# Kernel tuning notes

Measured on AMD Instinct MI355X. Metric: run time of the kernel, lower is better.

Reference implementation:

```python
import jax, jax.numpy as jnp
import numpy as np
from jax import lax

D_MODEL = 1024
N_HEADS = 8
D_HEAD = 64
D_INNER = N_HEADS * D_HEAD  # 512
B, T = 4, 4096
LN_EPS = 1e-5
NORM_EPS = 1e-12  # F.normalize default eps


def setup_inputs() -> dict:
    key = jax.random.key(0)
    ks = jax.random.split(key, 6)
    s_proj = (2.0 / (D_MODEL + D_INNER)) ** 0.5  # xavier_uniform-ish std
    x = jax.random.normal(ks[0], (B, T, D_MODEL), jnp.float32)
    Wq = jax.random.normal(ks[1], (D_MODEL, D_INNER), jnp.float32) * s_proj
    Wk = jax.random.normal(ks[2], (D_MODEL, D_INNER), jnp.float32) * s_proj
    Wv = jax.random.normal(ks[3], (D_MODEL, D_INNER), jnp.float32) * s_proj
    Wa = jax.random.normal(ks[4], (D_MODEL, D_INNER), jnp.float32) * s_proj
    ba = jnp.full((D_INNER,), 3.0, jnp.float32)  # nn.init.constant_(W_alpha.bias, 3.0)
    Wo = jax.random.normal(ks[5], (D_INNER, D_MODEL), jnp.float32) * s_proj
    gamma = jnp.ones((D_MODEL,), jnp.float32)
    beta = jnp.zeros((D_MODEL,), jnp.float32)
    return {"x": x, "Wq": Wq, "Wk": Wk, "Wv": Wv, "Wa": Wa, "ba": ba,
            "Wo": Wo, "gamma": gamma, "beta": beta}


def reference(x, Wq, Wk, Wv, Wa, ba, Wo, gamma, beta):
    Bx, Tx, _ = x.shape
    residual = x
    # LayerNorm
    mu = jnp.mean(x, axis=-1, keepdims=True)
    var = jnp.var(x, axis=-1, keepdims=True)
    xn = (x - mu) / jnp.sqrt(var + LN_EPS) * gamma + beta
    # Projections -> (B, T, H, d) -> time-major (T, B, H, d) for scan
    def heads(y):
        return jnp.moveaxis(y.reshape(Bx, Tx, N_HEADS, D_HEAD), 1, 0)
    q = heads(xn @ Wq)
    k = heads(xn @ Wk)
    v = heads(xn @ Wv)
    alpha = jax.nn.sigmoid(heads(xn @ Wa + ba))
    # F.normalize(k, dim=-1)
    knorm = jnp.linalg.norm(k, axis=-1, keepdims=True)
    k = k / jnp.maximum(knorm, NORM_EPS)

    # Recurrence: S_t = diag(a_t) S_{t-1} + k_t v_t^T ; o_t = S_t^T q_t
    def step(S, inp):
        q_t, k_t, v_t, a_t = inp  # each (B, H, d)
        S = a_t[..., None] * S + k_t[..., None] * v_t[..., None, :]  # (B,H,dk,dv)
        o_t = jnp.einsum('bhji,bhj->bhi', S, q_t)
        return S, o_t

    S0 = jnp.zeros((Bx, N_HEADS, D_HEAD, D_HEAD), x.dtype)
    _, outs = lax.scan(step, S0, (q, k, v, alpha))  # outs: (T, B, H, d)
    out = jnp.moveaxis(outs, 0, 1).reshape(Bx, Tx, D_INNER) @ Wo
    return out + residual
```

## Files before the change

kernel.cpp:

```cpp
#include <hip/hip_runtime.h>
#include <stdint.h>

#define NTOK   16384
#define DM     1024
#define DI     512
#define NH     8
#define DH     64
#define CHUNK  64
#define NCH    64
#define NBHC   2048

using short8 = __attribute__((ext_vector_type(8))) short;
using f32x4  = __attribute__((ext_vector_type(4))) float;

__device__ __forceinline__ unsigned short f2bf(float f) {
  union { float f; unsigned int u; } x; x.f = f;
  unsigned int u = x.u;
  return (unsigned short)((u + 0x7fffu + ((u >> 16) & 1u)) >> 16);
}
__device__ __forceinline__ float bf2f(unsigned short h) {
  union { unsigned int u; float f; } x; x.u = ((unsigned int)h) << 16; return x.f;
}

typedef const __attribute__((address_space(1))) void* gp1_t;
typedef __attribute__((address_space(3))) void* lp3_t;
__device__ __forceinline__ void gload_lds16(const void* g, void* l) {
  __builtin_amdgcn_global_load_lds((gp1_t)g, (lp3_t)l, 16, 0, 0);
}

__global__ __launch_bounds__(256) void init_kernel(const float* __restrict__ x,
                                                   const float* __restrict__ gamma,
                                                   const float* __restrict__ beta,
                                                   const float* __restrict__ Wq,
                                                   const float* __restrict__ Wk,
                                                   const float* __restrict__ Wv,
                                                   const float* __restrict__ Wa,
                                                   const float* __restrict__ Wo,
                                                   unsigned short* __restrict__ xn,
                                                   unsigned short* __restrict__ Wt,
                                                   unsigned short* __restrict__ Wot) {
  const int blk = blockIdx.x, tid = threadIdx.x;
  __shared__ float tile[32][33];
  __shared__ float rs_[4], rss_[4];
  if (blk < NTOK) {
    const int row = blk;
    float4 v = ((const float4*)(x + (long)row * DM))[tid];
    float s  = v.x + v.y + v.z + v.w;
    float ss = v.x * v.x + v.y * v.y + v.z * v.z + v.w * v.w;
    #pragma unroll
    for (int off = 32; off > 0; off >>= 1) { s += __shfl_down(s, off); ss += __shfl_down(ss, off); }
    int wave = tid >> 6, lane = tid & 63;
    if (lane == 0) { rs_[wave] = s; rss_[wave] = ss; }
    __syncthreads();
    s  = rs_[0] + rs_[1] + rs_[2] + rs_[3];
    ss = rss_[0] + rss_[1] + rss_[2] + rss_[3];
    float mu   = s * (1.f / DM);
    float var  = ss * (1.f / DM) - mu * mu;
    float rstd = rsqrtf(var + 1e-5f);
    int idx = tid * 4;
    float xv[4] = {v.x, v.y, v.z, v.w};
    unsigned short o[4];
    #pragma unroll
    for (int j = 0; j < 4; ++j) o[j] = f2bf((xv[j] - mu) * rstd * gamma[idx + j] + beta[idx + j]);
    uint2 pk; pk.x = (unsigned)o[0] | ((unsigned)o[1] << 16); pk.y = (unsigned)o[2] | ((unsigned)o[3] << 16);
    *(uint2*)(xn + (long)row * DM + idx) = pk;
  } else if (blk < NTOK + 2048) {
    const int id = blk - NTOK;
    const int z = id >> 9, r9 = id & 511;
    const float* in = (z == 0) ? Wq : (z == 1) ? Wk : (z == 2) ? Wv : Wa;
    unsigned short* o = Wt + (size_t)z * 512 * 1024;
    int bx = (r9 & 15) * 32, by = (r9 >> 4) * 32;
    int tx = tid & 31, ty = tid >> 5;
    #pragma unroll
    for (int r = ty; r < 32; r += 8) tile[r][tx] = in[(long)(by + r) * 512 + bx + tx];
    __syncthreads();
    #pragma unroll
    for (int r = ty; r < 32; r += 8) o[(long)(bx + r) * 1024 + by + tx] = f2bf(tile[tx][r]);
  } else {
    const int id = blk - NTOK - 2048;
    int bx = (id & 31) * 32, by = (id >> 5) * 32;
    int tx = tid & 31, ty = tid >> 5;
    #pragma unroll
    for (int r = ty; r < 32; r += 8) tile[r][tx] = Wo[(long)(by + r) * 1024 + bx + tx];
    __syncthreads();
    #pragma unroll
    for (int r = ty; r < 32; r += 8) Wot[(long)(bx + r) * 512 + by + tx] = f2bf(tile[tx][r]);
  }
}

#define EPS 136
template <int MODE>
__global__ __launch_bounds__(512) void gemm_bt(const unsigned short* __restrict__ A,
                                               const unsigned short* __restrict__ Bt,
                                               unsigned short* __restrict__ Cb,
                                               float* __restrict__ Cf,
                                               const float* __restrict__ resid,
                                               int M, int N, int K) {
  __shared__ __align__(16) unsigned short smem[128 * EPS];
  unsigned short* As = smem;
  unsigned short* Bs = smem + 8192;
  const int tid = threadIdx.x;
  const int wave = tid >> 6, lane = tid & 63;
  const int quad = lane >> 4, l16 = lane & 15;

  const int Nt = gridDim.y;
  int id = blockIdx.x + blockIdx.y * gridDim.x;
  int group = id / (4 * Nt);
  int rem = id - group * (4 * Nt);
  const int m0 = (group * 4 + (rem & 3)) * 256;
  const int n0 = (rem >> 2) * 128;
  const int wm = (wave & 3) * 64, wn = (wave >> 2) * 64;

  const int r4 = tid >> 2, p4 = (tid & 3) * 8;
  const unsigned short* Ag0 = A + (long)(m0 + r4) * K + p4;
  const unsigned short* Ag1 = A + (long)(m0 + 128 + r4) * K + p4;
  const unsigned short* Bg0 = Bt + (long)(n0 + r4) * K + p4;

  f32x4 acc[4][4];
  #pragma unroll
  for (int i = 0; i < 4; ++i)
    #pragma unroll
    for (int j = 0; j < 4; ++j) acc[i][j] = (f32x4){0.f, 0.f, 0.f, 0.f};

  for (int k0 = 0; k0 < K; k0 += 32) {
    __syncthreads();
    gload_lds16(Ag0 + k0, &As[tid * 8]);
    gload_lds16(Ag1 + k0, &As[(tid + 512) * 8]);
    gload_lds16(Bg0 + k0, &Bs[tid * 8]);
    __syncthreads();
    short8 a[4], b[4];
    #pragma unroll
    for (int mt = 0; mt < 4; ++mt) a[mt] = *(const short8*)&As[(wm + mt * 16 + l16) * 32 + quad * 8];
    #pragma unroll
    for (int nt = 0; nt < 4; ++nt) b[nt] = *(const short8*)&Bs[(wn + nt * 16 + l16) * 32 + quad * 8];
    #pragma unroll
    for (int mt = 0; mt < 4; ++mt)
      #pragma unroll
      for (int nt = 0; nt < 4; ++nt)
        acc[mt][nt] = __builtin_amdgcn_mfma_f32_16x16x32_bf16(a[mt], b[nt], acc[mt][nt], 0, 0, 0);
  }
  unsigned short* epi = smem;
  const int mypass = (wave & 3) >> 1;
  const int rloc = ((wave & 1) * 64);
  #pragma unroll
  for (int h = 0; h < 2; ++h) {
    __syncthreads();
    if (mypass == h) {
      #pragma unroll
      for (int mt = 0; mt < 4; ++mt)
        #pragma unroll
        for (int nt = 0; nt < 4; ++nt)
          #pragma unroll
          for (int r = 0; r < 4; ++r)
            epi[(rloc + mt * 16 + quad * 4 + r) * EPS + wn + nt * 16 + l16] = f2bf(acc[mt][nt][r]);
    }
    __syncthreads();
    if (MODE == 0) {
      #pragma unroll
      for (int i = tid; i < 2048; i += 512) {
        int row = i >> 4, cc = (i & 15) * 8;
        uint4 v = *(const uint4*)&epi[row * EPS + cc];
        *(uint4*)&Cb[(long)(m0 + h * 128 + row) * N + n0 + cc] = v;
      }
    } else {
      #pragma unroll
      for (int i = tid; i < 4096; i += 512) {
        int row = i >> 5, cc = (i & 31) * 4;
        long g = (long)(m0 + h * 128 + row) * N + n0 + cc;
        float4 rv = *(const float4*)&resid[g];
        uint2 pv = *(const uint2*)&epi[row * EPS + cc];
        float4 ov;
        ov.x = bf2f((unsigned short)(pv.x & 0xffffu)) + rv.x;
        ov.y = bf2f((unsigned short)(pv.x >> 16))     + rv.y;
        ov.z = bf2f((unsigned short)(pv.y & 0xffffu)) + rv.z;
        ov.w = bf2f((unsigned short)(pv.y >> 16))     + rv.w;
        *(float4*)&Cf[g] = ov;
      }
    }
  }
}

#define TS 72
__global__ __launch_bounds__(256) void prep_intra_kernel(const unsigned short* __restrict__ Cb,
                                                         const float* __restrict__ ba,
                                                         unsigned short* __restrict__ qt,
                                                         float* __restrict__ Dvec,
                                                         unsigned short* __restrict__ Ointra,
                                                         unsigned short* __restrict__ Tt) {
  const int bhc = blockIdx.x;
  const int c = bhc & 63, bh = bhc >> 6;
  const int h = bh & 7, b = bh >> 3;
  const int tid = threadIdx.x;
  __shared__ __align__(16) unsigned short Qb[4096], Kb[4096], Vb[4096], lamB[4096];
  __shared__ __align__(16) unsigned short Vt[64 * TS], Kt[64 * TS];
  __shared__ float rnF[64], lendF[64];
  const long rowbase = ((long)(b * 4096 + c * 64)) * 2048;
  const int hoff = h * 64;

  if (tid < 64) rnF[tid] = 0.f;
  __syncthreads();

  #pragma unroll
  for (int chunk = 0; chunk < 2; ++chunk) {
    int u = chunk * 256 + tid;
    int t = u >> 3, p = u & 7;
    long g = rowbase + (long)t * 2048 + hoff + p * 8;
    uint4 q4 = *(const uint4*)(Cb + g);
    uint4 k4 = *(const uint4*)(Cb + g + 512);
    uint4 v4 = *(const uint4*)(Cb + g + 1024);
    uint4 a4 = *(const uint4*)(Cb + g + 1536);
    *(uint4*)&Qb[u * 8] = q4;
    *(uint4*)&Kb[u * 8] = k4;
    *(uint4*)&Vb[u * 8] = v4;
    const unsigned short* as_ = (const unsigned short*)&a4;
    unsigned short al[8];
    #pragma unroll
    for (int j = 0; j < 8; ++j) {
      float z = bf2f(as_[j]) + ba[hoff + p * 8 + j];
      al[j] = f2bf(1.f / (1.f + __expf(-z)));
    }
    uint4 pa;
    pa.x = (unsigned)al[0] | ((unsigned)al[1] << 16); pa.y = (unsigned)al[2] | ((unsigned)al[3] << 16);
    pa.z = (unsigned)al[4] | ((unsigned)al[5] << 16); pa.w = (unsigned)al[6] | ((unsigned)al[7] << 16);
    *(uint4*)&lamB[u * 8] = pa;
    const unsigned short* ks = (const unsigned short*)&k4;
    float ssq = 0.f;
    #pragma unroll
    for (int j = 0; j < 8; ++j) { float kv = bf2f(ks[j]); ssq += kv * kv; }
    atomicAdd(&rnF[t], ssq);
  }
  __syncthreads();

  if (tid < 64) {
    int d = tid; float cum = 1.f;
    #pragma unroll
    for (int t = 0; t < 64; ++t) {
      cum *= bf2f(lamB[t * 64 + d]);
      lamB[t * 64 + d] = f2bf(cum);
    }
    Dvec[(long)bhc * 64 + d] = cum;
    lendF[d] = cum;
  } else if (tid < 128) {
    int t = tid - 64;
    rnF[t] = 1.f / fmaxf(sqrtf(rnF[t]), 1e-12f);
  }
  __syncthreads();

  #pragma unroll
  for (int j = 0; j < 16; ++j) {
    int e = j * 256 + tid;
    int t = e >> 6;
    float lam = bf2f(lamB[e]);
    float kn = bf2f(Kb[e]) * rnF[t];
    Qb[e] = f2bf(bf2f(Qb[e]) * lam);
    Kb[e] = f2bf(kn / lam);
  }
  __syncthreads();

  {
    const long obase = (long)bhc * 4096;
    uint4* gq = (uint4*)(qt + obase);
    const uint4* lq = (const uint4*)Qb;
    gq[tid] = lq[tid]; gq[tid + 256] = lq[tid + 256];
  }

  const long base = (long)bhc * 4096;
  const int wave = tid >> 6, lane = tid & 63, quad = lane >> 4, l16 = lane & 15;
  const int mrow = wave * 16 + l16;
  unsigned short* Ps = lamB;

  union { short8 v; short s[8]; } aI;
  aI.v = (short8){0,0,0,0,0,0,0,0};
  {
    int target = ((wave & 1) * 16 + l16) - quad * 8;
    if (target >= 0 && target < 8) aI.s[target] = (short)0x3F80;
  }
  const int bsel = (wave >> 1) * 32;

  {
    short8 a0 = *(const short8*)&Qb[mrow * 64 + quad * 8];
    short8 a1 = *(const short8*)&Qb[mrow * 64 + 32 + quad * 8];
    #pragma unroll
    for (int nt = 0; nt < 4; ++nt) {
      short8 b0 = *(const short8*)&Kb[(nt * 16 + l16) * 64 + quad * 8];
      short8 b1 = *(const short8*)&Kb[(nt * 16 + l16) * 64 + 32 + quad * 8];
      f32x4 acc = (f32x4){0.f, 0.f, 0.f, 0.f};
      acc = __builtin_amdgcn_mfma_f32_16x16x32_bf16(a0, b0, acc, 0, 0, 0);
      acc = __builtin_amdgcn_mfma_f32_16x16x32_bf16(a1, b1, acc, 0, 0, 0);
      #pragma unroll
      for (int r = 0; r < 4; ++r) {
        int t = wave * 16 + quad * 4 + r, u = nt * 16 + l16;
        Ps[t * 64 + u] = (u <= t) ? f2bf(acc[r]) : (unsigned short)0;
      }
    }
  }
  #pragma unroll
  for (int nt = 0; nt < 4; ++nt) {
    short8 bv = *(const short8*)&Vb[(nt * 16 + l16) * 64 + bsel + quad * 8];
    short8 bk = *(const short8*)&Kb[(nt * 16 + l16) * 64 + bsel + quad * 8];
    f32x4 av = (f32x4){0.f, 0.f, 0.f, 0.f};
    f32x4 ak = (f32x4){0.f, 0.f, 0.f, 0.f};
    av = __builtin_amdgcn_mfma_f32_16x16x32_bf16(aI.v, bv, av, 0, 0, 0);
    ak = __builtin_amdgcn_mfma_f32_16x16x32_bf16(aI.v, bk, ak, 0, 0, 0);
    #pragma unroll
    for (int r = 0; r < 4; ++r) {
      int i = wave * 16 + quad * 4 + r, t = nt * 16 + l16;
      Vt[i * TS + t] = f2bf(av[r]);
      Kt[i * TS + t] = f2bf(ak[r]);
    }
  }
  __syncthreads();

  {
    short8 a0 = *(const short8*)&Ps[mrow * 64 + quad * 8];
    short8 a1 = *(const short8*)&Ps[mrow * 64 + 32 + quad * 8];
    #pragma unroll
    for (int nt = 0; nt < 4; ++nt) {
      short8 b0 = *(const short8*)&Vt[(nt * 16 + l16) * TS + quad * 8];
      short8 b1 = *(const short8*)&Vt[(nt * 16 + l16) * TS + 32 + quad * 8];
      f32x4 acc = (f32x4){0.f, 0.f, 0.f, 0.f};
      acc = __builtin_amdgcn_mfma_f32_16x16x32_bf16(a0, b0, acc, 0, 0, 0);
      acc = __builtin_amdgcn_mfma_f32_16x16x32_bf16(a1, b1, acc, 0, 0, 0);
      #pragma unroll
      for (int r = 0; r < 4; ++r) {
        int t = wave * 16 + quad * 4 + r, i = nt * 16 + l16;
        Ointra[base + t * 64 + i] = f2bf(acc[r]);
      }
    }
  }
  {
    short8 a0 = *(const short8*)&Vt[mrow * TS + quad * 8];
    short8 a1 = *(const short8*)&Vt[mrow * TS + 32 + quad * 8];
    #pragma unroll
    for (int nt = 0; nt < 4; ++nt) {
      short8 b0 = *(const short8*)&Kt[(nt * 16 + l16) * TS + quad * 8];
      short8 b1 = *(const short8*)&Kt[(nt * 16 + l16) * TS + 32 + quad * 8];
      f32x4 acc = (f32x4){0.f, 0.f, 0.f, 0.f};
      acc = __builtin_amdgcn_mfma_f32_16x16x32_bf16(a0, b0, acc, 0, 0, 0);
      acc = __builtin_amdgcn_mfma_f32_16x16x32_bf16(a1, b1, acc, 0, 0, 0);
      float le = lendF[nt * 16 + l16];
      #pragma unroll
      for (int r = 0; r < 4; ++r) {
        int i = wave * 16 + quad * 4 + r, j = nt * 16 + l16;
        Tt[base + i * 64 + j] = f2bf(acc[r] * le);
      }
    }
  }
}

__global__ __launch_bounds__(256) void scan_kernel(const unsigned short* __restrict__ Tt,
                                                   const float* __restrict__ Dvec,
                                                   unsigned short* __restrict__ Sst) {
  const int bh = blockIdx.x;
  const int e = blockIdx.y * 256 + threadIdx.x;
  const int j = e & 63;
  float S = 0.f;
  for (int c = 0; c < 64; ++c) {
    const long idx = ((long)(bh * 64 + c)) * 4096 + e;
    const float dj = Dvec[((long)(bh * 64 + c)) * 64 + j];
    Sst[idx] = f2bf(S);
    S = dj * S + bf2f(Tt[idx]);
  }
}

__global__ __launch_bounds__(256) void combine_kernel(const unsigned short* __restrict__ qt,
                                                      const unsigned short* __restrict__ Sst,
                                                      const unsigned short* __restrict__ Ointra,
                                                      unsigned short* __restrict__ O) {
  const int bhc = blockIdx.x;
  const int c = bhc & 63, bh = bhc >> 6;
  const int h = bh & 7, b = bh >> 3;
  const long base = (long)bhc * 4096;
  __shared__ __align__(16) unsigned short Qs[4096], Sb[4096];
  const int tid = threadIdx.x;
  {
    const uint4* gq = (const uint4*)(qt + base);  uint4* lq = (uint4*)Qs;
    const uint4* gs = (const uint4*)(Sst + base); uint4* ls = (uint4*)Sb;
    lq[tid] = gq[tid]; lq[tid + 256] = gq[tid + 256];
    ls[tid] = gs[tid]; ls[tid + 256] = gs[tid + 256];
  }
  __syncthreads();
  const int wave = tid >> 6, lane = tid & 63, quad = lane >> 4, l16 = lane & 15;
  const int mrow = wave * 16 + l16;
  short8 a0 = *(const short8*)&Qs[mrow * 64 + quad * 8];
  short8 a1 = *(const short8*)&Qs[mrow * 64 + 32 + quad * 8];
  #pragma unroll
  for (int nt = 0; nt < 4; ++nt) {
    f32x4 acc;
    #pragma unroll
    for (int r = 0; r < 4; ++r) {
      int t = wave * 16 + quad * 4 + r, i = nt * 16 + l16;
      acc[r] = bf2f(Ointra[base + t * 64 + i]);
    }
    short8 b0 = *(const short8*)&Sb[(nt * 16 + l16) * 64 + quad * 8];
    short8 b1 = *(const short8*)&Sb[(nt * 16 + l16) * 64 + 32 + quad * 8];
    acc = __builtin_amdgcn_mfma_f32_16x16x32_bf16(a0, b0, acc, 0, 0, 0);
    acc = __builtin_amdgcn_mfma_f32_16x16x32_bf16(a1, b1, acc, 0, 0, 0);
    #pragma unroll
    for (int r = 0; r < 4; ++r) {
      int t = wave * 16 + quad * 4 + r, i = nt * 16 + l16;
      O[((long)(b * 4096 + c * 64 + t)) * 512 + h * 64 + i] = f2bf(acc[r]);
    }
  }
}

extern "C" void kernel_launch(void* const* d_in, const int* in_sizes, int n_in,
                              void* d_out, int out_size, void* d_ws, size_t ws_size,
                              hipStream_t stream) {
  const float* x     = (const float*)d_in[0];
  const float* Wq    = (const float*)d_in[1];
  const float* Wk    = (const float*)d_in[2];
  const float* Wv    = (const float*)d_in[3];
  const float* Wa    = (const float*)d_in[4];
  const float* ba    = (const float*)d_in[5];
  const float* Wo    = (const float*)d_in[6];
  const float* gamma = (const float*)d_in[7];
  const float* beta  = (const float*)d_in[8];
  float* out = (float*)d_out;

  char* ws = (char*)d_ws;
  const size_t KB = 1024;
  unsigned short* Wt     = (unsigned short*)(ws + 0 * KB);
  unsigned short* Wot    = (unsigned short*)(ws + 4096 * KB);
  float*          Dvec   = (float*)         (ws + 5120 * KB);
  unsigned short* qt     = (unsigned short*)(ws + 5632 * KB);
  unsigned short* Ttb    = (unsigned short*)(ws + 22016 * KB);
  unsigned short* Sst    = (unsigned short*)(ws + 38400 * KB);
  unsigned short* xn     = (unsigned short*)(ws + 54784 * KB);
  unsigned short* Ointra = (unsigned short*)(ws + 54784 * KB);
  unsigned short* Ob     = (unsigned short*)(ws + 71168 * KB);
  unsigned short* Cb     = (unsigned short*)(ws + 87552 * KB);

  init_kernel<<<NTOK + 2048 + 512, 256, 0, stream>>>(x, gamma, beta, Wq, Wk, Wv, Wa, Wo, xn, Wt, Wot);
  gemm_bt<0><<<dim3(NTOK / 256, 2048 / 128), 512, 0, stream>>>(xn, Wt, Cb, nullptr, nullptr, NTOK, 2048, 1024);
  prep_intra_kernel<<<NBHC, 256, 0, stream>>>(Cb, ba, qt, Dvec, Ointra, Ttb);
  scan_kernel<<<dim3(32, 16), 256, 0, stream>>>(Ttb, Dvec, Sst);
  combine_kernel<<<NBHC, 256, 0, stream>>>(qt, Sst, Ointra, Ob);
  gemm_bt<1><<<dim3(NTOK / 256, 1024 / 128), 512, 0, stream>>>(Ob, Wot, nullptr, out, x, NTOK, 1024, 512);
}
```

Baseline: 308.4 us.

## Replace GEMM with 256x256 double-buffered swizzled-LDS pipelined MFMA kernel

```diff
diff --git a/kernel.cpp b/kernel.cpp
--- a/kernel.cpp
+++ b/kernel.cpp
@@ -88,87 +88,175 @@
   }
 }
 
-#define EPS 136
+#define EPSW 264
 template <int MODE>
-__global__ __launch_bounds__(512) void gemm_bt(const unsigned short* __restrict__ A,
-                                               const unsigned short* __restrict__ Bt,
-                                               unsigned short* __restrict__ Cb,
-                                               float* __restrict__ Cf,
-                                               const float* __restrict__ resid,
-                                               int M, int N, int K) {
-  __shared__ __align__(16) unsigned short smem[128 * EPS];
-  unsigned short* As = smem;
-  unsigned short* Bs = smem + 8192;
+__global__ __launch_bounds__(512, 2) void gemm8(const unsigned short* __restrict__ A,
+                                                const unsigned short* __restrict__ Bt,
+                                                unsigned short* __restrict__ Cb,
+                                                float* __restrict__ Cf,
+                                                const float* __restrict__ resid,
+                                                int M, int N, int K) {
+  __shared__ __align__(16) unsigned short sm[65536];
   const int tid = threadIdx.x;
   const int wave = tid >> 6, lane = tid & 63;
   const int quad = lane >> 4, l16 = lane & 15;
-
-  const int Nt = gridDim.y;
-  int id = blockIdx.x + blockIdx.y * gridDim.x;
-  int group = id / (4 * Nt);
-  int rem = id - group * (4 * Nt);
-  const int m0 = (group * 4 + (rem & 3)) * 256;
-  const int n0 = (rem >> 2) * 128;
-  const int wm = (wave & 3) * 64, wn = (wave >> 2) * 64;
-
-  const int r4 = tid >> 2, p4 = (tid & 3) * 8;
-  const unsigned short* Ag0 = A + (long)(m0 + r4) * K + p4;
-  const unsigned short* Ag1 = A + (long)(m0 + 128 + r4) * K + p4;
-  const unsigned short* Bg0 = Bt + (long)(n0 + r4) * K + p4;
-
-  f32x4 acc[4][4];
-  #pragma unroll
-  for (int i = 0; i < 4; ++i)
+  const int wm = wave >> 2, wn = wave & 3;
+
+  const int nwg = gridDim.x;
+  const int cpx = nwg >> 3;
+  const int bid = blockIdx.x;
+  const int swz = (bid & 7) * cpx + (bid >> 3);
+  const int m0 = (swz & 63) * 256;
+  const int n0 = (swz >> 6) * 256;
+
+  const int rloc = tid >> 3;
+  const int cbu = ((((tid & 7) << 4) ^ ((rloc & 7) << 4)) >> 1);
+  const unsigned short* ap = A + (long)(m0 + rloc) * K + cbu;
+  const unsigned short* bp = Bt + (long)(n0 + rloc) * K + cbu;
+  const int dst = tid * 8;
+
+  const int colu0 = (((quad << 4) ^ ((l16 & 7) << 4)) >> 1);
+  const int colu1 = colu0 ^ 32;
+  const int aoff = (wm * 128 + l16) * 64;
+  const int boff = 16384 + (wn * 64 + l16) * 64;
+
+  f32x4 acc[8][4];
+  #pragma unroll
+  for (int i = 0; i < 8; ++i)
     #pragma unroll
     for (int j = 0; j < 4; ++j) acc[i][j] = (f32x4){0.f, 0.f, 0.f, 0.f};
 
-  for (int k0 = 0; k0 < K; k0 += 32) {
-    __syncthreads();
-    gload_lds16(Ag0 + k0, &As[tid * 8]);
-    gload_lds16(Ag1 + k0, &As[(tid + 512) * 8]);
-    gload_lds16(Bg0 + k0, &Bs[tid * 8]);
-    __syncthreads();
-    short8 a[4], b[4];
-    #pragma unroll
-    for (int mt = 0; mt < 4; ++mt) a[mt] = *(const short8*)&As[(wm + mt * 16 + l16) * 32 + quad * 8];
-    #pragma unroll
-    for (int nt = 0; nt < 4; ++nt) b[nt] = *(const short8*)&Bs[(wn + nt * 16 + l16) * 32 + quad * 8];
+  const int NT = K >> 6;
+
+  #pragma unroll
+  for (int u = 0; u < 4; ++u) {
+    gload_lds16(ap + (long)u * 64 * K, &sm[u * 4096 + dst]);
+    gload_lds16(bp + (long)u * 64 * K, &sm[16384 + u * 4096 + dst]);
+  }
+  asm volatile("s_waitcnt vmcnt(0)" ::: "memory");
+  __builtin_amdgcn_s_barrier();
+  __builtin_amdgcn_sched_barrier(0);
+
+  short8 aR[4][2];
+  short8 bR[2][2][2];
+
+  for (int t = 0; t < NT; ++t) {
+    const unsigned short* sc = sm + (t & 1) * 32768;
+    unsigned short* sn = sm + ((t + 1) & 1) * 32768;
+    const unsigned short* apn = ap + (long)(t + 1) * 64;
+    const unsigned short* bpn = bp + (long)(t + 1) * 64;
+    const bool more = (t + 1 < NT);
+
+    #pragma unroll
+    for (int mt = 0; mt < 4; ++mt) {
+      aR[mt][0] = *(const short8*)&sc[aoff + mt * 1024 + colu0];
+      aR[mt][1] = *(const short8*)&sc[aoff + mt * 1024 + colu1];
+    }
+    #pragma unroll
+    for (int nt = 0; nt < 2; ++nt) {
+      bR[0][nt][0] = *(const short8*)&sc[boff + nt * 1024 + colu0];
+      bR[0][nt][1] = *(const short8*)&sc[boff + nt * 1024 + colu1];
+    }
+    if (more) {
+      gload_lds16(apn,                  &sn[dst]);
+      gload_lds16(apn + (long) 64 * K,  &sn[4096 + dst]);
+      gload_lds16(apn + (long)128 * K,  &sn[8192 + dst]);
+      gload_lds16(apn + (long)192 * K,  &sn[12288 + dst]);
+    }
+    __builtin_amdgcn_s_barrier();
+    __builtin_amdgcn_s_setprio(1);
     #pragma unroll
     for (int mt = 0; mt < 4; ++mt)
       #pragma unroll
-      for (int nt = 0; nt < 4; ++nt)
-        acc[mt][nt] = __builtin_amdgcn_mfma_f32_16x16x32_bf16(a[mt], b[nt], acc[mt][nt], 0, 0, 0);
-  }
-  unsigned short* epi = smem;
-  const int mypass = (wave & 3) >> 1;
-  const int rloc = ((wave & 1) * 64);
+      for (int nt = 0; nt < 2; ++nt) {
+        acc[mt][nt] = __builtin_amdgcn_mfma_f32_16x16x32_bf16(aR[mt][0], bR[0][nt][0], acc[mt][nt], 0, 0, 0);
+        acc[mt][nt] = __builtin_amdgcn_mfma_f32_16x16x32_bf16(aR[mt][1], bR[0][nt][1], acc[mt][nt], 0, 0, 0);
+      }
+    __builtin_amdgcn_s_setprio(0);
+    __builtin_amdgcn_s_barrier();
+
+    #pragma unroll
+    for (int nt = 0; nt < 2; ++nt) {
+      bR[1][nt][0] = *(const short8*)&sc[boff + (nt + 2) * 1024 + colu0];
+      bR[1][nt][1] = *(const short8*)&sc[boff + (nt + 2) * 1024 + colu1];
+    }
+    if (more) {
+      gload_lds16(bpn,                  &sn[16384 + dst]);
+      gload_lds16(bpn + (long) 64 * K,  &sn[16384 + 4096 + dst]);
+      gload_lds16(bpn + (long)128 * K,  &sn[16384 + 8192 + dst]);
+      gload_lds16(bpn + (long)192 * K,  &sn[16384 + 12288 + dst]);
+    }
+    __builtin_amdgcn_s_barrier();
+    __builtin_amdgcn_s_setprio(1);
+    #pragma unroll
+    for (int mt = 0; mt < 4; ++mt)
+      #pragma unroll
+      for (int nt = 0; nt < 2; ++nt) {
+        acc[mt][nt + 2] = __builtin_amdgcn_mfma_f32_16x16x32_bf16(aR[mt][0], bR[1][nt][0], acc[mt][nt + 2], 0, 0, 0);
+        acc[mt][nt + 2] = __builtin_amdgcn_mfma_f32_16x16x32_bf16(aR[mt][1], bR[1][nt][1], acc[mt][nt + 2], 0, 0, 0);
+      }
+    __builtin_amdgcn_s_setprio(0);
+    __builtin_amdgcn_s_barrier();
+
+    #pragma unroll
+    for (int mt = 0; mt < 4; ++mt) {
+      aR[mt][0] = *(const short8*)&sc[aoff + 4096 + mt * 1024 + colu0];
+      aR[mt][1] = *(const short8*)&sc[aoff + 4096 + mt * 1024 + colu1];
+    }
+    __builtin_amdgcn_s_barrier();
+    __builtin_amdgcn_s_setprio(1);
+    #pragma unroll
+    for (int mt = 0; mt < 4; ++mt)
+      #pragma unroll
+      for (int nt = 0; nt < 2; ++nt) {
+        acc[4 + mt][nt + 2] = __builtin_amdgcn_mfma_f32_16x16x32_bf16(aR[mt][0], bR[1][nt][0], acc[4 + mt][nt + 2], 0, 0, 0);
+        acc[4 + mt][nt + 2] = __builtin_amdgcn_mfma_f32_16x16x32_bf16(aR[mt][1], bR[1][nt][1], acc[4 + mt][nt + 2], 0, 0, 0);
+      }
+    __builtin_amdgcn_s_setprio(0);
+    __builtin_amdgcn_s_barrier();
+
+    __builtin_amdgcn_s_barrier();
+    __builtin_amdgcn_s_setprio(1);
+    #pragma unroll
+    for (int mt = 0; mt < 4; ++mt)
+      #pragma unroll
+      for (int nt = 0; nt < 2; ++nt) {
+        acc[4 + mt][nt] = __builtin_amdgcn_mfma_f32_16x16x32_bf16(aR[mt][0], bR[0][nt][0], acc[4 + mt][nt], 0, 0, 0);
+        acc[4 + mt][nt] = __builtin_amdgcn_mfma_f32_16x16x32_bf16(aR[mt][1], bR[0][nt][1], acc[4 + mt][nt], 0, 0, 0);
+      }
+    __builtin_amdgcn_s_setprio(0);
+    if (more) asm volatile("s_waitcnt vmcnt(0)" ::: "memory");
+    __builtin_amdgcn_s_barrier();
+    __builtin_amdgcn_sched_barrier(0);
+  }
+
+  unsigned short* epi = sm;
   #pragma unroll
   for (int h = 0; h < 2; ++h) {
-    __syncthreads();
-    if (mypass == h) {
-      #pragma unroll
-      for (int mt = 0; mt < 4; ++mt)
+    if (wm == h) {
+      #pragma unroll
+      for (int fm = 0; fm < 8; ++fm)
         #pragma unroll
-        for (int nt = 0; nt < 4; ++nt)
+        for (int fn = 0; fn < 4; ++fn)
           #pragma unroll
           for (int r = 0; r < 4; ++r)
-            epi[(rloc + mt * 16 + quad * 4 + r) * EPS + wn + nt * 16 + l16] = f2bf(acc[mt][nt][r]);
+            epi[(fm * 16 + quad * 4 + r) * EPSW + wn * 64 + fn * 16 + l16] = f2bf(acc[fm][fn][r]);
     }
     __syncthreads();
     if (MODE == 0) {
       #pragma unroll
-      for (int i = tid; i < 2048; i += 512) {
-        int row = i >> 4, cc = (i & 15) * 8;
-        uint4 v = *(const uint4*)&epi[row * EPS + cc];
+      for (int i = tid; i < 4096; i += 512) {
+        int row = i >> 5, cc = (i & 31) * 8;
+        uint4 v = *(const uint4*)&epi[row * EPSW + cc];
         *(uint4*)&Cb[(long)(m0 + h * 128 + row) * N + n0 + cc] = v;
       }
     } else {
       #pragma unroll
-      for (int i = tid; i < 4096; i += 512) {
-        int row = i >> 5, cc = (i & 31) * 4;
+      for (int i = tid; i < 8192; i += 512) {
+        int row = i >> 6, cc = (i & 63) * 4;
         long g = (long)(m0 + h * 128 + row) * N + n0 + cc;
         float4 rv = *(const float4*)&resid[g];
-        uint2 pv = *(const uint2*)&epi[row * EPS + cc];
+        uint2 pv = *(const uint2*)&epi[row * EPSW + cc];
         float4 ov;
         ov.x = bf2f((unsigned short)(pv.x & 0xffffu)) + rv.x;
         ov.y = bf2f((unsigned short)(pv.x >> 16))     + rv.y;
@@ -177,6 +265,7 @@
         *(float4*)&Cf[g] = ov;
       }
     }
+    __syncthreads();
   }
 }
 
@@ -432,9 +521,9 @@
   unsigned short* Cb     = (unsigned short*)(ws + 87552 * KB);
 
   init_kernel<<<NTOK + 2048 + 512, 256, 0, stream>>>(x, gamma, beta, Wq, Wk, Wv, Wa, Wo, xn, Wt, Wot);
-  gemm_bt<0><<<dim3(NTOK / 256, 2048 / 128), 512, 0, stream>>>(xn, Wt, Cb, nullptr, nullptr, NTOK, 2048, 1024);
+  gemm8<0><<<512, 512, 0, stream>>>(xn, Wt, Cb, nullptr, nullptr, NTOK, 2048, 1024);
   prep_intra_kernel<<<NBHC, 256, 0, stream>>>(Cb, ba, qt, Dvec, Ointra, Ttb);
   scan_kernel<<<dim3(32, 16), 256, 0, stream>>>(Ttb, Dvec, Sst);
   combine_kernel<<<NBHC, 256, 0, stream>>>(qt, Sst, Ointra, Ob);
-  gemm_bt<1><<<dim3(NTOK / 256, 1024 / 128), 512, 0, stream>>>(Ob, Wot, nullptr, out, x, NTOK, 1024, 512);
-}
+  gemm8<1><<<256, 512, 0, stream>>>(Ob, Wot, nullptr, out, x, NTOK, 1024, 512);
+}
```

After: 311.4 us. Within noise of the previous version (+1.0%).

## Rewrite projection GEMMs with 256x256 tiles, 4-stage LDS pipeline and swizzle

Applied to the files above, without the earlier changes.

```diff
diff --git a/kernel.cpp b/kernel.cpp
--- a/kernel.cpp
+++ b/kernel.cpp
@@ -88,87 +88,122 @@
   }
 }
 
-#define EPS 136
+#define EPSW 264
+#define G4_TILE(T_, DOSTAGE_, WAITC_)                                         \
+  {                                                                           \
+    if (DOSTAGE_) {                                                           \
+      const int s_ = (T_) + 3;                                                \
+      unsigned short* sb_ = &sm[(s_ & 3) * 16384];                            \
+      const long ko_ = (long)s_ * 32;                                         \
+      gload_lds16(a0p + ko_, sb_ + dst);                                      \
+      gload_lds16(a1p + ko_, sb_ + 4096 + dst);                               \
+      gload_lds16(b0p + ko_, sb_ + 8192 + dst);                               \
+      gload_lds16(b1p + ko_, sb_ + 12288 + dst);                              \
+    }                                                                         \
+    const unsigned short* cb_ = &sm[((T_) & 3) * 16384];                      \
+    short8 av_[8], bv_[4];                                                    \
+    _Pragma("unroll")                                                         \
+    for (int mt = 0; mt < 8; ++mt) av_[mt] = *(const short8*)&cb_[aoff + mt * 512]; \
+    _Pragma("unroll")                                                         \
+    for (int nt = 0; nt < 4; ++nt) bv_[nt] = *(const short8*)&cb_[boff + nt * 512]; \
+    __builtin_amdgcn_s_setprio(1);                                            \
+    _Pragma("unroll")                                                         \
+    for (int mt = 0; mt < 8; ++mt)                                            \
+      _Pragma("unroll")                                                       \
+      for (int nt = 0; nt < 4; ++nt)                                          \
+        acc[mt][nt] = __builtin_amdgcn_mfma_f32_16x16x32_bf16(av_[mt], bv_[nt], acc[mt][nt], 0, 0, 0); \
+    __builtin_amdgcn_s_setprio(0);                                            \
+    asm volatile("s_waitcnt " WAITC_ ::: "memory");                           \
+    __builtin_amdgcn_s_barrier();                                             \
+    __builtin_amdgcn_sched_barrier(0);                                        \
+  }
+
 template <int MODE>
-__global__ __launch_bounds__(512) void gemm_bt(const unsigned short* __restrict__ A,
-                                               const unsigned short* __restrict__ Bt,
-                                               unsigned short* __restrict__ Cb,
-                                               float* __restrict__ Cf,
-                                               const float* __restrict__ resid,
-                                               int M, int N, int K) {
-  __shared__ __align__(16) unsigned short smem[128 * EPS];
-  unsigned short* As = smem;
-  unsigned short* Bs = smem + 8192;
+__global__ __launch_bounds__(512, 2) void gemm4s(const unsigned short* __restrict__ A,
+                                                 const unsigned short* __restrict__ Bt,
+                                                 unsigned short* __restrict__ Cb,
+                                                 float* __restrict__ Cf,
+                                                 const float* __restrict__ resid,
+                                                 int M, int N, int K) {
+  __shared__ __align__(16) unsigned short sm[65536];
   const int tid = threadIdx.x;
   const int wave = tid >> 6, lane = tid & 63;
   const int quad = lane >> 4, l16 = lane & 15;
-
-  const int Nt = gridDim.y;
-  int id = blockIdx.x + blockIdx.y * gridDim.x;
-  int group = id / (4 * Nt);
-  int rem = id - group * (4 * Nt);
-  const int m0 = (group * 4 + (rem & 3)) * 256;
-  const int n0 = (rem >> 2) * 128;
-  const int wm = (wave & 3) * 64, wn = (wave >> 2) * 64;
-
-  const int r4 = tid >> 2, p4 = (tid & 3) * 8;
-  const unsigned short* Ag0 = A + (long)(m0 + r4) * K + p4;
-  const unsigned short* Ag1 = A + (long)(m0 + 128 + r4) * K + p4;
-  const unsigned short* Bg0 = Bt + (long)(n0 + r4) * K + p4;
-
-  f32x4 acc[4][4];
-  #pragma unroll
-  for (int i = 0; i < 4; ++i)
+  const int wm = wave >> 2, wn = wave & 3;
+
+  const int nwg = gridDim.x;
+  const int cpx = nwg >> 3;
+  const int bid = blockIdx.x;
+  const int swz = (bid & 7) * cpx + (bid >> 3);
+  const int m0 = (swz & 63) * 256;
+  const int n0 = (swz >> 6) * 256;
+
+  const int r2 = tid >> 2;
+  const int scol = ((tid & 3) * 8) ^ (((tid >> 3) & 3) * 8);
+  const unsigned short* a0p = A + (long)(m0 + r2) * K + scol;
+  const unsigned short* a1p = A + (long)(m0 + 128 + r2) * K + scol;
+  const unsigned short* b0p = Bt + (long)(n0 + r2) * K + scol;
+  const unsigned short* b1p = Bt + (long)(n0 + 128 + r2) * K + scol;
+  const int dst = tid * 8;
+
+  const int swzr = (quad * 8) ^ (((l16 >> 1) & 3) * 8);
+  const int aoff = (wm * 128 + l16) * 32 + swzr;
+  const int boff = 8192 + (wn * 64 + l16) * 32 + swzr;
+
+  f32x4 acc[8][4];
+  #pragma unroll
+  for (int i = 0; i < 8; ++i)
     #pragma unroll
     for (int j = 0; j < 4; ++j) acc[i][j] = (f32x4){0.f, 0.f, 0.f, 0.f};
 
-  for (int k0 = 0; k0 < K; k0 += 32) {
-    __syncthreads();
-    gload_lds16(Ag0 + k0, &As[tid * 8]);
-    gload_lds16(Ag1 + k0, &As[(tid + 512) * 8]);
-    gload_lds16(Bg0 + k0, &Bs[tid * 8]);
-    __syncthreads();
-    short8 a[4], b[4];
-    #pragma unroll
-    for (int mt = 0; mt < 4; ++mt) a[mt] = *(const short8*)&As[(wm + mt * 16 + l16) * 32 + quad * 8];
-    #pragma unroll
-    for (int nt = 0; nt < 4; ++nt) b[nt] = *(const short8*)&Bs[(wn + nt * 16 + l16) * 32 + quad * 8];
-    #pragma unroll
-    for (int mt = 0; mt < 4; ++mt)
-      #pragma unroll
-      for (int nt = 0; nt < 4; ++nt)
-        acc[mt][nt] = __builtin_amdgcn_mfma_f32_16x16x32_bf16(a[mt], b[nt], acc[mt][nt], 0, 0, 0);
-  }
-  unsigned short* epi = smem;
-  const int mypass = (wave & 3) >> 1;
-  const int rloc = ((wave & 1) * 64);
+  const int NT = K >> 5;
+
+  #pragma unroll
+  for (int s = 0; s < 3; ++s) {
+    unsigned short* sb = &sm[s * 16384];
+    const long ko = (long)s * 32;
+    gload_lds16(a0p + ko, sb + dst);
+    gload_lds16(a1p + ko, sb + 4096 + dst);
+    gload_lds16(b0p + ko, sb + 8192 + dst);
+    gload_lds16(b1p + ko, sb + 12288 + dst);
+  }
+  asm volatile("s_waitcnt vmcnt(8)" ::: "memory");
+  __builtin_amdgcn_s_barrier();
+  __builtin_amdgcn_sched_barrier(0);
+
+  int t = 0;
+  for (; t < NT - 3; ++t) G4_TILE(t, true, "vmcnt(8)");
+  G4_TILE(t, false, "vmcnt(4)"); ++t;
+  G4_TILE(t, false, "vmcnt(0)"); ++t;
+  G4_TILE(t, false, "vmcnt(0)");
+
+  unsigned short* epi = sm;
   #pragma unroll
   for (int h = 0; h < 2; ++h) {
-    __syncthreads();
-    if (mypass == h) {
-      #pragma unroll
-      for (int mt = 0; mt < 4; ++mt)
+    if (wm == h) {
+      #pragma unroll
+      for (int fm = 0; fm < 8; ++fm)
         #pragma unroll
-        for (int nt = 0; nt < 4; ++nt)
+        for (int fn = 0; fn < 4; ++fn)
           #pragma unroll
           for (int r = 0; r < 4; ++r)
-            epi[(rloc + mt * 16 + quad * 4 + r) * EPS + wn + nt * 16 + l16] = f2bf(acc[mt][nt][r]);
+            epi[(fm * 16 + quad * 4 + r) * EPSW + wn * 64 + fn * 16 + l16] = f2bf(acc[fm][fn][r]);
     }
     __syncthreads();
     if (MODE == 0) {
       #pragma unroll
-      for (int i = tid; i < 2048; i += 512) {
-        int row = i >> 4, cc = (i & 15) * 8;
-        uint4 v = *(const uint4*)&epi[row * EPS + cc];
+      for (int i = tid; i < 4096; i += 512) {
+        int row = i >> 5, cc = (i & 31) * 8;
+        uint4 v = *(const uint4*)&epi[row * EPSW + cc];
         *(uint4*)&Cb[(long)(m0 + h * 128 + row) * N + n0 + cc] = v;
       }
     } else {
       #pragma unroll
-      for (int i = tid; i < 4096; i += 512) {
-        int row = i >> 5, cc = (i & 31) * 4;
+      for (int i = tid; i < 8192; i += 512) {
+        int row = i >> 6, cc = (i & 63) * 4;
         long g = (long)(m0 + h * 128 + row) * N + n0 + cc;
         float4 rv = *(const float4*)&resid[g];
-        uint2 pv = *(const uint2*)&epi[row * EPS + cc];
+        uint2 pv = *(const uint2*)&epi[row * EPSW + cc];
         float4 ov;
         ov.x = bf2f((unsigned short)(pv.x & 0xffffu)) + rv.x;
         ov.y = bf2f((unsigned short)(pv.x >> 16))     + rv.y;
@@ -177,6 +212,7 @@
         *(float4*)&Cf[g] = ov;
       }
     }
+    __syncthreads();
   }
 }
 
@@ -432,9 +468,9 @@
   unsigned short* Cb     = (unsigned short*)(ws + 87552 * KB);
 
   init_kernel<<<NTOK + 2048 + 512, 256, 0, stream>>>(x, gamma, beta, Wq, Wk, Wv, Wa, Wo, xn, Wt, Wot);
-  gemm_bt<0><<<dim3(NTOK / 256, 2048 / 128), 512, 0, stream>>>(xn, Wt, Cb, nullptr, nullptr, NTOK, 2048, 1024);
+  gemm4s<0><<<512, 512, 0, stream>>>(xn, Wt, Cb, nullptr, nullptr, NTOK, 2048, 1024);
   prep_intra_kernel<<<NBHC, 256, 0, stream>>>(Cb, ba, qt, Dvec, Ointra, Ttb);
   scan_kernel<<<dim3(32, 16), 256, 0, stream>>>(Ttb, Dvec, Sst);
   combine_kernel<<<NBHC, 256, 0, stream>>>(qt, Sst, Ointra, Ob);
-  gemm_bt<1><<<dim3(NTOK / 256, 1024 / 128), 512, 0, stream>>>(Ob, Wot, nullptr, out, x, NTOK, 1024, 512);
-}
+  gemm4s<1><<<256, 512, 0, stream>>>(Ob, Wot, nullptr, out, x, NTOK, 1024, 512);
+}
```

Measured after the change: 312.9 us. Within noise of the previous version (+1.4%).
